# Kernel optimization log

Measured on AMD Instinct MI355X. Metric: run time of the kernel, lower is better.

## Reference

```python
import jax, jax.numpy as jnp
import numpy as np

B = 65536
QUERY_DIM = 1024
CROSS_DIM = 1024
HEADS = 16
DIM_HEAD = 64
INNER = HEADS * DIM_HEAD  # 1024
SCALE = DIM_HEAD ** -0.5


def setup_inputs() -> dict:
    key = jax.random.key(0)
    ks = jax.random.split(key, 7)
    s_in = 1.0 / np.sqrt(QUERY_DIM)
    s_c = 1.0 / np.sqrt(CROSS_DIM)
    s_o = 1.0 / np.sqrt(INNER)
    return {
        "latent": jax.random.normal(ks[0], (B, QUERY_DIM), jnp.float32),
        "cond_latent": jax.random.normal(ks[1], (B, CROSS_DIM), jnp.float32),
        "Wq": jax.random.normal(ks[2], (INNER, QUERY_DIM), jnp.float32) * s_in,
        "Wk": jax.random.normal(ks[3], (INNER, CROSS_DIM), jnp.float32) * s_c,
        "Wv": jax.random.normal(ks[4], (INNER, CROSS_DIM), jnp.float32) * s_c,
        "Wout": jax.random.normal(ks[5], (QUERY_DIM, INNER), jnp.float32) * s_o,
        "bout": jax.random.normal(ks[6], (QUERY_DIM,), jnp.float32) * s_o,
    }


def reference(latent, cond_latent, Wq, Wk, Wv, Wout, bout):
    # projections: [B, inner] -> [B, heads, dim_head]
    Q = (latent @ Wq.T).reshape(B, HEADS, DIM_HEAD)
    K = (cond_latent @ Wk.T).reshape(B, HEADS, DIM_HEAD)
    V = (cond_latent @ Wv.T).reshape(B, HEADS, DIM_HEAD)
    # attention across the heads axis: scores [B, heads, heads]
    scores = jnp.einsum("bhd,bgd->bhg", Q, K) * SCALE
    probs = jax.nn.softmax(scores, axis=-1)
    feats = jnp.einsum("bhg,bgd->bhd", probs, V).reshape(B, INNER)
    return feats @ Wout.T + bout
```

## Files before the change

### kernel.cpp

```cpp
#include <hip/hip_runtime.h>
#include <hip/hip_bf16.h>

#define NB    65536
#define KDIM  1024
#define NDIM  1024

#define BM 128
#define BN 128
#define BK 32
#define NT (KDIM / BK)

typedef float f32x4  __attribute__((ext_vector_type(4)));
typedef short short8 __attribute__((ext_vector_type(8)));
typedef unsigned short ushort8v __attribute__((ext_vector_type(8)));

static __device__ __forceinline__ unsigned short f2bf(float f) {
    union { float f; unsigned u; } v; v.f = f;
    unsigned r = v.u + 0x7FFFu + ((v.u >> 16) & 1u);
    return (unsigned short)(r >> 16);
}
static __device__ __forceinline__ float bf2f(unsigned short h) {
    union { unsigned u; float f; } v; v.u = ((unsigned)h) << 16;
    return v.f;
}

static __device__ __forceinline__ void gload16(const unsigned short* g, unsigned short* l) {
    __builtin_amdgcn_global_load_lds(
        (const __attribute__((address_space(1))) unsigned int*)g,
        (__attribute__((address_space(3))) unsigned int*)l, 16, 0, 0);
}


__global__ __launch_bounds__(256) void pack_f32_k(
    const float* __restrict__ src, unsigned short* __restrict__ dst)
{
    const int tid = threadIdx.x;
    const int r   = blockIdx.x * 16 + (tid >> 4);
    const int cb  = (tid & 15) * 64;
    const int p   = r >> 8;
    const int f   = (r >> 4) & 15;
    const int rl  = r & 15;
    const float* s = src + (size_t)r * 1024 + cb;
#pragma unroll
    for (int g = 0; g < 8; ++g) {
        float4 va = *reinterpret_cast<const float4*>(s + g * 8);
        float4 vb = *reinterpret_cast<const float4*>(s + g * 8 + 4);
        ushort8v o;
        o[0] = f2bf(va.x); o[1] = f2bf(va.y); o[2] = f2bf(va.z); o[3] = f2bf(va.w);
        o[4] = f2bf(vb.x); o[5] = f2bf(vb.y); o[6] = f2bf(vb.z); o[7] = f2bf(vb.w);
        const int c0 = cb + g * 8;
        const int t  = c0 >> 5;
        const int kc = (c0 & 31) >> 3;
        *reinterpret_cast<ushort8v*>(
            &dst[((size_t)(p * 32 + t) * 16 + f) * 512 + kc * 128 + rl * 8]) = o;
    }
}

template<int OUT_F32, int NN>
__global__ __launch_bounds__(256, 4) void gemm128(
    const unsigned short* __restrict__ Ap, const unsigned short* __restrict__ Wp,
    const float* __restrict__ bias, void* __restrict__ Cptr)
{
    constexpr int GN = NN / BN;
    __shared__ alignas(16) unsigned short lds[2][2][8][512];

    const int t    = threadIdx.x;
    const int lane = t & 63;
    const int wid  = t >> 6;
    const int wm   = wid >> 1;
    const int wn   = wid & 1;

    const int nwg  = gridDim.x;
    const int cpx  = nwg >> 3;
    const int orig = blockIdx.x;
    const int wgid = (orig & 7) * cpx + (orig >> 3);
    const int bn0  = (wgid & (GN - 1)) * BN;
    const int bm0  = (wgid / GN) * BM;

    const int pA  = bm0 >> 8;  const int f0A = (bm0 >> 4) & 15;
    const int pB  = bn0 >> 8;  const int f0B = (bn0 >> 4) & 15;

#define STAGE_(TAU, SLOT) do {                                                  \
        int _tc = (TAU) < NT ? (TAU) : NT - 1;                                  \
        _Pragma("unroll")                                                       \
        for (int _ab = 0; _ab < 2; ++_ab) {                                     \
            const unsigned short* _b = _ab ? Wp : Ap;                           \
            int _pp = _ab ? pB : pA;                                            \
            int _f0 = _ab ? f0B : f0A;                                          \
            _Pragma("unroll")                                                   \
            for (int _j = 0; _j < 2; ++_j) {                                    \
                int _f = wid * 2 + _j;                                          \
                gload16(_b + ((size_t)(_pp * 32 + _tc) * 16 + _f0 + _f) * 512 + lane * 8, \
                        &lds[SLOT][_ab][_f][0]);                                \
            }                                                                   \
        }                                                                       \
    } while (0)

    f32x4 acc[4][4];
#pragma unroll
    for (int mi = 0; mi < 4; ++mi)
#pragma unroll
        for (int ni = 0; ni < 4; ++ni)
            acc[mi][ni] = (f32x4){0.f, 0.f, 0.f, 0.f};

    STAGE_(0, 0);
    asm volatile("s_waitcnt vmcnt(0)" ::: "memory");
    __builtin_amdgcn_s_barrier();

#pragma unroll 1
    for (int tt = 0; tt < NT; ++tt) {
        const int slot = tt & 1;
        if (tt + 1 < NT) STAGE_(tt + 1, slot ^ 1);

        short8 af[4], bq[4];
#pragma unroll
        for (int mi = 0; mi < 4; ++mi)
            af[mi] = *reinterpret_cast<const short8*>(&lds[slot][0][wm * 4 + mi][lane * 8]);
#pragma unroll
        for (int ni = 0; ni < 4; ++ni)
            bq[ni] = *reinterpret_cast<const short8*>(&lds[slot][1][wn * 4 + ni][lane * 8]);
        __builtin_amdgcn_s_setprio(1);
#pragma unroll
        for (int mi = 0; mi < 4; ++mi)
#pragma unroll
            for (int ni = 0; ni < 4; ++ni)
                acc[mi][ni] = __builtin_amdgcn_mfma_f32_16x16x32_bf16(
                    af[mi], bq[ni], acc[mi][ni], 0, 0, 0);
        __builtin_amdgcn_s_setprio(0);
        asm volatile("s_waitcnt vmcnt(0)" ::: "memory");
        __builtin_amdgcn_s_barrier();
    }

    const int crow = (lane >> 4) * 4;
    const int ccol = lane & 15;

    if (OUT_F32) {
        float* Cf  = (float*)Cptr;
        float* bbf = reinterpret_cast<float*>(&lds[0][0][0][0]);
        float bv[4];
#pragma unroll
        for (int ni = 0; ni < 4; ++ni)
            bv[ni] = bias[bn0 + wn * 64 + ni * 16 + ccol];
#pragma unroll
        for (int p = 0; p < 4; ++p) {
            if (wm == (p >> 1)) {
#pragma unroll
                for (int mlo = 0; mlo < 2; ++mlo) {
                    int ml = (p & 1) * 2 + mlo;
#pragma unroll
                    for (int ni = 0; ni < 4; ++ni)
#pragma unroll
                        for (int r = 0; r < 4; ++r)
                            bbf[(mlo * 16 + crow + r) * 136 + wn * 64 + ni * 16 + ccol]
                                = acc[ml][ni][r] + bv[ni];
                }
            }
            __syncthreads();
#pragma unroll
            for (int it = 0; it < 4; ++it) {
                int lrow = it * 8 + (t >> 5);
                int lcol = (t & 31) * 4;
                f32x4 v = *reinterpret_cast<const f32x4*>(&bbf[lrow * 136 + lcol]);
                *reinterpret_cast<f32x4*>(
                    &Cf[(size_t)(bm0 + p * 32 + lrow) * NN + bn0 + lcol]) = v;
            }
            __syncthreads();
        }
    } else {
        unsigned short* Cb = (unsigned short*)Cptr;
        unsigned short* bb = &lds[0][0][0][0];
#pragma unroll
        for (int p = 0; p < 2; ++p) {
            if (wm == p) {
#pragma unroll
                for (int ml = 0; ml < 4; ++ml)
#pragma unroll
                    for (int ni = 0; ni < 4; ++ni)
#pragma unroll
                        for (int r = 0; r < 4; ++r)
                            bb[(ml * 16 + crow + r) * 136 + wn * 64 + ni * 16 + ccol]
                                = f2bf(acc[ml][ni][r]);
            }
            __syncthreads();
#pragma unroll
            for (int it = 0; it < 4; ++it) {
                int lrow = it * 16 + (t >> 4);
                int lcol = (t & 15) * 8;
                ushort8v v = *reinterpret_cast<const ushort8v*>(&bb[lrow * 136 + lcol]);
                *reinterpret_cast<ushort8v*>(
                    &Cb[(size_t)(bm0 + p * 64 + lrow) * NN + bn0 + lcol]) = v;
            }
            __syncthreads();
        }
    }
#undef STAGE_
}

__global__ __launch_bounds__(1024) void attn_k(
    const unsigned short* __restrict__ Qb, const unsigned short* __restrict__ KVb,
    unsigned short* __restrict__ Fp)
{
    __shared__ alignas(16) unsigned short KL[16][1024];
    __shared__ alignas(16) unsigned short VL[16][1024];
    const int t = threadIdx.x;
    const int lane = t & 63;
    const int wid = t >> 6;
    const size_t row = (size_t)blockIdx.x * 16 + wid;
    const size_t base = row * 1024;
    const size_t bkv  = row * 2048;
    const int off = lane * 16;

    ushort8v q0 = *reinterpret_cast<const ushort8v*>(&Qb[base + off]);
    ushort8v q1 = *reinterpret_cast<const ushort8v*>(&Qb[base + off + 8]);
    float qf[16];
#pragma unroll
    for (int j = 0; j < 8; ++j) { qf[j] = bf2f(q0[j]); qf[8 + j] = bf2f(q1[j]); }

    *reinterpret_cast<ushort8v*>(&KL[wid][off])     = *reinterpret_cast<const ushort8v*>(&KVb[bkv + off]);
    *reinterpret_cast<ushort8v*>(&KL[wid][off + 8]) = *reinterpret_cast<const ushort8v*>(&KVb[bkv + off + 8]);
    *reinterpret_cast<ushort8v*>(&VL[wid][off])     = *reinterpret_cast<const ushort8v*>(&KVb[bkv + 1024 + off]);
    *reinterpret_cast<ushort8v*>(&VL[wid][off + 8]) = *reinterpret_cast<const ushort8v*>(&KVb[bkv + 1024 + off + 8]);
    __syncthreads();

    const int sub = lane & 3;
    float s[16];
#pragma unroll
    for (int g = 0; g < 16; ++g) {
        const ushort8v k0 = *reinterpret_cast<const ushort8v*>(&KL[wid][g * 64 + sub * 16]);
        const ushort8v k1 = *reinterpret_cast<const ushort8v*>(&KL[wid][g * 64 + sub * 16 + 8]);
        float acc = 0.f;
#pragma unroll
        for (int j = 0; j < 8; ++j)
            acc += qf[j] * bf2f(k0[j]) + qf[8 + j] * bf2f(k1[j]);
        s[g] = acc;
    }
#pragma unroll
    for (int m = 1; m <= 2; m <<= 1)
#pragma unroll
        for (int g = 0; g < 16; ++g)
            s[g] += __shfl_xor(s[g], m, 64);

    float mx = s[0];
#pragma unroll
    for (int g = 1; g < 16; ++g) mx = fmaxf(mx, s[g]);
    float p[16], denom = 0.f;
#pragma unroll
    for (int g = 0; g < 16; ++g) {
        p[g] = __expf((s[g] - mx) * 0.125f);
        denom += p[g];
    }
    float inv = 1.f / denom;

    float f[16];
#pragma unroll
    for (int j = 0; j < 16; ++j) f[j] = 0.f;
#pragma unroll
    for (int g = 0; g < 16; ++g) {
        float pg = p[g] * inv;
        const ushort8v v0 = *reinterpret_cast<const ushort8v*>(&VL[wid][g * 64 + sub * 16]);
        const ushort8v v1 = *reinterpret_cast<const ushort8v*>(&VL[wid][g * 64 + sub * 16 + 8]);
#pragma unroll
        for (int j = 0; j < 8; ++j) {
            f[j]     += pg * bf2f(v0[j]);
            f[8 + j] += pg * bf2f(v1[j]);
        }
    }
    ushort8v o0, o1;
#pragma unroll
    for (int j = 0; j < 8; ++j) { o0[j] = f2bf(f[j]); o1[j] = f2bf(f[8 + j]); }
    *reinterpret_cast<ushort8v*>(&KL[wid][off])     = o0;
    *reinterpret_cast<ushort8v*>(&KL[wid][off + 8]) = o1;
    __syncthreads();

    const int r0 = blockIdx.x * 16;
    const int pp = r0 >> 8;
    const int ff = (r0 >> 4) & 15;
    const int tt = t >> 5;
    const int kc = (t >> 3) & 3;
    const int rp = t & 7;
    unsigned short* db = &Fp[((size_t)(pp * 32 + tt) * 16 + ff) * 512 + kc * 128 + rp * 16];
    *reinterpret_cast<ushort8v*>(db)     = *reinterpret_cast<const ushort8v*>(&KL[rp * 2][tt * 32 + kc * 8]);
    *reinterpret_cast<ushort8v*>(db + 8) = *reinterpret_cast<const ushort8v*>(&KL[rp * 2 + 1][tt * 32 + kc * 8]);
}

extern "C" void kernel_launch(void* const* d_in, const int* in_sizes, int n_in,
                              void* d_out, int out_size, void* d_ws, size_t ws_size,
                              hipStream_t stream)
{
    (void)in_sizes; (void)n_in; (void)out_size; (void)ws_size;
    const float* latent = (const float*)d_in[0];
    const float* cond   = (const float*)d_in[1];
    const float* Wq     = (const float*)d_in[2];
    const float* Wk     = (const float*)d_in[3];
    const float* Wv     = (const float*)d_in[4];
    const float* Wout   = (const float*)d_in[5];
    const float* bout   = (const float*)d_in[6];
    float* out = (float*)d_out;

    char* ws = (char*)d_ws;
    const size_t MB = 1ull << 20;
    unsigned short* wqp  = (unsigned short*)(ws + 0 * MB);
    unsigned short* wkvp = (unsigned short*)(ws + 2 * MB);
    unsigned short* wop  = (unsigned short*)(ws + 6 * MB);
    unsigned short* Qb   = (unsigned short*)(ws + 8 * MB);
    unsigned short* KVb  = (unsigned short*)(ws + 136 * MB);
    unsigned short* Lp   = (unsigned short*)(ws + 392 * MB);
    unsigned short* Cp   = (unsigned short*)(ws + 520 * MB);
    unsigned short* Fp   = Lp;

    pack_f32_k<<<NDIM / 16, 256, 0, stream>>>(Wq,   wqp);
    pack_f32_k<<<NDIM / 16, 256, 0, stream>>>(Wk,   wkvp);
    pack_f32_k<<<NDIM / 16, 256, 0, stream>>>(Wv,   wkvp + 1048576);
    pack_f32_k<<<NDIM / 16, 256, 0, stream>>>(Wout, wop);

    pack_f32_k<<<NB / 16, 256, 0, stream>>>(latent, Lp);
    pack_f32_k<<<NB / 16, 256, 0, stream>>>(cond,   Cp);

    gemm128<0, 1024><<<(NB / 128) * (1024 / 128), 256, 0, stream>>>(Lp, wqp,  nullptr, Qb);
    gemm128<0, 2048><<<(NB / 128) * (2048 / 128), 256, 0, stream>>>(Cp, wkvp, nullptr, KVb);

    attn_k<<<NB / 16, 1024, 0, stream>>>(Qb, KVb, Fp);

    gemm128<1, 1024><<<(NB / 128) * (1024 / 128), 256, 0, stream>>>(Fp, wop, bout, out);
}
```

Baseline: 1.046 ms.

## Load GEMM fragments directly from global into registers, enlarge tile to 256x128

```diff
diff --git a/kernel.cpp b/kernel.cpp
--- a/kernel.cpp
+++ b/kernel.cpp
@@ -5,8 +5,6 @@
 #define KDIM  1024
 #define NDIM  1024
 
-#define BM 128
-#define BN 128
 #define BK 32
 #define NT (KDIM / BK)
 
@@ -22,12 +20,6 @@
 static __device__ __forceinline__ float bf2f(unsigned short h) {
     union { unsigned u; float f; } v; v.u = ((unsigned)h) << 16;
     return v.f;
-}
-
-static __device__ __forceinline__ void gload16(const unsigned short* g, unsigned short* l) {
-    __builtin_amdgcn_global_load_lds(
-        (const __attribute__((address_space(1))) unsigned int*)g,
-        (__attribute__((address_space(3))) unsigned int*)l, 16, 0, 0);
 }
 
 
@@ -57,12 +49,12 @@
 }
 
 template<int OUT_F32, int NN>
-__global__ __launch_bounds__(256, 4) void gemm128(
+__global__ __launch_bounds__(256, 2) void gemm_rs(
     const unsigned short* __restrict__ Ap, const unsigned short* __restrict__ Wp,
     const float* __restrict__ bias, void* __restrict__ Cptr)
 {
-    constexpr int GN = NN / BN;
-    __shared__ alignas(16) unsigned short lds[2][2][8][512];
+    constexpr int GN = NN / 128;
+    __shared__ alignas(16) unsigned short bounce[64 * 136];
 
     const int t    = threadIdx.x;
     const int lane = t & 63;
@@ -74,61 +66,53 @@
     const int cpx  = nwg >> 3;
     const int orig = blockIdx.x;
     const int wgid = (orig & 7) * cpx + (orig >> 3);
-    const int bn0  = (wgid & (GN - 1)) * BN;
-    const int bm0  = (wgid / GN) * BM;
-
-    const int pA  = bm0 >> 8;  const int f0A = (bm0 >> 4) & 15;
+    const int bn0  = (wgid & (GN - 1)) * 128;
+    const int bm0  = (wgid / GN) * 256;
+
+    const int pA  = bm0 >> 8;
     const int pB  = bn0 >> 8;  const int f0B = (bn0 >> 4) & 15;
 
-#define STAGE_(TAU, SLOT) do {                                                  \
-        int _tc = (TAU) < NT ? (TAU) : NT - 1;                                  \
+    const unsigned short* baseA = Ap + ((size_t)pA * 32 * 16 + wm * 8) * 512 + lane * 8;
+    const unsigned short* baseB = Wp + ((size_t)pB * 32 * 16 + f0B + wn * 4) * 512 + lane * 8;
+
+#define LOADT_(T, AA, BB) do {                                                  \
         _Pragma("unroll")                                                       \
-        for (int _ab = 0; _ab < 2; ++_ab) {                                     \
-            const unsigned short* _b = _ab ? Wp : Ap;                           \
-            int _pp = _ab ? pB : pA;                                            \
-            int _f0 = _ab ? f0B : f0A;                                          \
+        for (int _mi = 0; _mi < 8; ++_mi)                                       \
+            AA[_mi] = *reinterpret_cast<const short8*>(                         \
+                baseA + (size_t)(T) * 8192 + _mi * 512);                        \
+        _Pragma("unroll")                                                       \
+        for (int _ni = 0; _ni < 4; ++_ni)                                       \
+            BB[_ni] = *reinterpret_cast<const short8*>(                         \
+                baseB + (size_t)(T) * 8192 + _ni * 512);                        \
+    } while (0)
+
+#define MFMA_(AA, BB) do {                                                      \
+        __builtin_amdgcn_s_setprio(1);                                          \
+        _Pragma("unroll")                                                       \
+        for (int _mi = 0; _mi < 8; ++_mi)                                       \
             _Pragma("unroll")                                                   \
-            for (int _j = 0; _j < 2; ++_j) {                                    \
-                int _f = wid * 2 + _j;                                          \
-                gload16(_b + ((size_t)(_pp * 32 + _tc) * 16 + _f0 + _f) * 512 + lane * 8, \
-                        &lds[SLOT][_ab][_f][0]);                                \
-            }                                                                   \
-        }                                                                       \
+            for (int _ni = 0; _ni < 4; ++_ni)                                   \
+                acc[_mi][_ni] = __builtin_amdgcn_mfma_f32_16x16x32_bf16(        \
+                    AA[_mi], BB[_ni], acc[_mi][_ni], 0, 0, 0);                  \
+        __builtin_amdgcn_s_setprio(0);                                          \
     } while (0)
 
-    f32x4 acc[4][4];
-#pragma unroll
-    for (int mi = 0; mi < 4; ++mi)
+    f32x4 acc[8][4];
+#pragma unroll
+    for (int mi = 0; mi < 8; ++mi)
 #pragma unroll
         for (int ni = 0; ni < 4; ++ni)
             acc[mi][ni] = (f32x4){0.f, 0.f, 0.f, 0.f};
 
-    STAGE_(0, 0);
-    asm volatile("s_waitcnt vmcnt(0)" ::: "memory");
-    __builtin_amdgcn_s_barrier();
+    short8 a0[8], b0[4], a1[8], b1[4];
+    LOADT_(0, a0, b0);
 
 #pragma unroll 1
-    for (int tt = 0; tt < NT; ++tt) {
-        const int slot = tt & 1;
-        if (tt + 1 < NT) STAGE_(tt + 1, slot ^ 1);
-
-        short8 af[4], bq[4];
-#pragma unroll
-        for (int mi = 0; mi < 4; ++mi)
-            af[mi] = *reinterpret_cast<const short8*>(&lds[slot][0][wm * 4 + mi][lane * 8]);
-#pragma unroll
-        for (int ni = 0; ni < 4; ++ni)
-            bq[ni] = *reinterpret_cast<const short8*>(&lds[slot][1][wn * 4 + ni][lane * 8]);
-        __builtin_amdgcn_s_setprio(1);
-#pragma unroll
-        for (int mi = 0; mi < 4; ++mi)
-#pragma unroll
-            for (int ni = 0; ni < 4; ++ni)
-                acc[mi][ni] = __builtin_amdgcn_mfma_f32_16x16x32_bf16(
-                    af[mi], bq[ni], acc[mi][ni], 0, 0, 0);
-        __builtin_amdgcn_s_setprio(0);
-        asm volatile("s_waitcnt vmcnt(0)" ::: "memory");
-        __builtin_amdgcn_s_barrier();
+    for (int tt = 0; tt < NT; tt += 2) {
+        LOADT_(tt + 1, a1, b1);
+        MFMA_(a0, b0);
+        if (tt + 2 < NT) LOADT_(tt + 2, a0, b0);
+        MFMA_(a1, b1);
     }
 
     const int crow = (lane >> 4) * 4;
@@ -136,17 +120,17 @@
 
     if (OUT_F32) {
         float* Cf  = (float*)Cptr;
-        float* bbf = reinterpret_cast<float*>(&lds[0][0][0][0]);
+        float* bbf = reinterpret_cast<float*>(&bounce[0]);
         float bv[4];
 #pragma unroll
         for (int ni = 0; ni < 4; ++ni)
             bv[ni] = bias[bn0 + wn * 64 + ni * 16 + ccol];
 #pragma unroll
-        for (int p = 0; p < 4; ++p) {
-            if (wm == (p >> 1)) {
+        for (int p = 0; p < 8; ++p) {
+            if (wm == (p >> 2)) {
 #pragma unroll
                 for (int mlo = 0; mlo < 2; ++mlo) {
-                    int ml = (p & 1) * 2 + mlo;
+                    int ml = (p & 3) * 2 + mlo;
 #pragma unroll
                     for (int ni = 0; ni < 4; ++ni)
 #pragma unroll
@@ -168,32 +152,34 @@
         }
     } else {
         unsigned short* Cb = (unsigned short*)Cptr;
-        unsigned short* bb = &lds[0][0][0][0];
-#pragma unroll
-        for (int p = 0; p < 2; ++p) {
-            if (wm == p) {
-#pragma unroll
-                for (int ml = 0; ml < 4; ++ml)
+#pragma unroll
+        for (int p = 0; p < 4; ++p) {
+            if (wm == (p >> 1)) {
+#pragma unroll
+                for (int mlj = 0; mlj < 4; ++mlj) {
+                    int ml = (p & 1) * 4 + mlj;
 #pragma unroll
                     for (int ni = 0; ni < 4; ++ni)
 #pragma unroll
                         for (int r = 0; r < 4; ++r)
-                            bb[(ml * 16 + crow + r) * 136 + wn * 64 + ni * 16 + ccol]
+                            bounce[(mlj * 16 + crow + r) * 136 + wn * 64 + ni * 16 + ccol]
                                 = f2bf(acc[ml][ni][r]);
+                }
             }
             __syncthreads();
 #pragma unroll
             for (int it = 0; it < 4; ++it) {
                 int lrow = it * 16 + (t >> 4);
                 int lcol = (t & 15) * 8;
-                ushort8v v = *reinterpret_cast<const ushort8v*>(&bb[lrow * 136 + lcol]);
+                ushort8v v = *reinterpret_cast<const ushort8v*>(&bounce[lrow * 136 + lcol]);
                 *reinterpret_cast<ushort8v*>(
                     &Cb[(size_t)(bm0 + p * 64 + lrow) * NN + bn0 + lcol]) = v;
             }
             __syncthreads();
         }
     }
-#undef STAGE_
+#undef LOADT_
+#undef MFMA_
 }
 
 __global__ __launch_bounds__(1024) void attn_k(
@@ -316,10 +302,10 @@
     pack_f32_k<<<NB / 16, 256, 0, stream>>>(latent, Lp);
     pack_f32_k<<<NB / 16, 256, 0, stream>>>(cond,   Cp);
 
-    gemm128<0, 1024><<<(NB / 128) * (1024 / 128), 256, 0, stream>>>(Lp, wqp,  nullptr, Qb);
-    gemm128<0, 2048><<<(NB / 128) * (2048 / 128), 256, 0, stream>>>(Cp, wkvp, nullptr, KVb);
+    gemm_rs<0, 1024><<<(NB / 256) * (1024 / 128), 256, 0, stream>>>(Lp, wqp,  nullptr, Qb);
+    gemm_rs<0, 2048><<<(NB / 256) * (2048 / 128), 256, 0, stream>>>(Cp, wkvp, nullptr, KVb);
 
     attn_k<<<NB / 16, 1024, 0, stream>>>(Qb, KVb, Fp);
 
-    gemm128<1, 1024><<<(NB / 128) * (1024 / 128), 256, 0, stream>>>(Fp, wop, bout, out);
-}
+    gemm_rs<1, 1024><<<(NB / 256) * (1024 / 128), 256, 0, stream>>>(Fp, wop, bout, out);
+}
```

After: 1.082 ms. +3.5%, slower.
